# Kernel tuning notes

Hardware: AMD Instinct MI355X
Metric: run time of the kernel (lower is better)

## Reference

```python
import jax, jax.numpy as jnp
import numpy as np

EPS = 1e-10
COMMITMENT_COST = 0.25


def setup_inputs() -> dict:
    key = jax.random.key(0)
    k1, k2 = jax.random.split(key)
    inputs = jax.random.normal(k1, (64, 64, 32, 32), dtype=jnp.float32)
    # nn.init.uniform_(weight, -1.0, 1.0)
    embeddings = jax.random.uniform(k2, (1024, 64), dtype=jnp.float32, minval=-1.0, maxval=1.0)
    return {"inputs": inputs, "embeddings": embeddings}


def reference(inputs, embeddings):
    B, C, H, W = inputs.shape  # C == embedding_dim
    K = embeddings.shape[0]
    x = jnp.transpose(inputs, (0, 2, 3, 1)).reshape(-1, C)  # [N, D]
    d = (jnp.sum(x * x, axis=1, keepdims=True)
         - 2.0 * (x @ embeddings.T)
         + jnp.sum(embeddings * embeddings, axis=1))  # [N, K]
    idx = jnp.argmin(d, axis=1)  # [N]
    # one-hot @ embeddings == gather
    q = jnp.take(embeddings, idx, axis=0)  # [N, D]
    x4 = x.reshape(B, H, W, C)
    q4 = q.reshape(B, H, W, C)
    e_latent = jnp.mean((jax.lax.stop_gradient(q4) - x4) ** 2)
    q_latent = jnp.mean((q4 - jax.lax.stop_gradient(x4)) ** 2)
    loss = q_latent + COMMITMENT_COST * e_latent
    # straight-through estimator
    st = x4 + jax.lax.stop_gradient(q4 - x4)
    # avg_probs = mean of one-hot encodings == normalized histogram
    n = idx.shape[0]
    avg_probs = jnp.zeros((K,), dtype=jnp.float32).at[idx].add(1.0) / n
    perplexity = jnp.exp(-jnp.sum(avg_probs * jnp.log(avg_probs + EPS)))
    quantized = jnp.transpose(st, (0, 3, 1, 2))
    return quantized, loss, perplexity
```

## Files before the change

### kernel.cpp

```cpp
#include <hip/hip_runtime.h>

#define N_TOTAL   65536
#define HW_SZ     1024
#define CDIM      64
#define K_CODES   1024
#define OUT_ELEMS 4194304
#define QT        128
#define NCT       (K_CODES / 16)
#define TAU       0.004f


typedef __attribute__((ext_vector_type(8))) short short8;
typedef __attribute__((ext_vector_type(4))) float f32x4;

__device__ __forceinline__ unsigned short f2bf(float x) {
    unsigned u = __float_as_uint(x);
    return (unsigned short)((u + 0x7FFFu + ((u >> 16) & 1u)) >> 16);
}
__device__ __forceinline__ float bf2f(unsigned short h) {
    return __uint_as_float(((unsigned)h) << 16);
}
__device__ __forceinline__ void gload_lds16(const void* g, void* l) {
    __builtin_amdgcn_global_load_lds(
        (const __attribute__((address_space(1))) void*)g,
        (__attribute__((address_space(3))) void*)l, 16, 0, 0);
}

__global__ void k_prep(const float* __restrict__ emb, float* __restrict__ enorm,
                       short* __restrict__ btab, unsigned int* __restrict__ hist) {
    int gid = blockIdx.x * 256 + threadIdx.x;
    int r  = gid >> 4;
    int d0 = (gid & 15) * 4;
    float4 v = *(const float4*)(emb + gid * 4);
    float s = v.x * v.x + v.y * v.y + v.z * v.z + v.w * v.w;
#pragma unroll
    for (int off = 1; off < 16; off <<= 1) s += __shfl_xor(s, off, 64);
    if ((gid & 15) == 0) enorm[r] = s;

    float vv[4] = {v.x, v.y, v.z, v.w};
    short h[4], l[4];
#pragma unroll
    for (int j = 0; j < 4; ++j) {
        unsigned short hh = f2bf(vv[j]);
        h[j] = (short)hh;
        l[j] = (short)f2bf(vv[j] - bf2f(hh));
    }
    int base = (r >> 4) * 2048 + (d0 >> 5) * 1024
             + ((((d0 >> 3) & 3) * 16 + (r & 15)) * 8) + (d0 & 7);
    *(short4*)&btab[base]       = make_short4(h[0], h[1], h[2], h[3]);
    *(short4*)&btab[base + 512] = make_short4(l[0], l[1], l[2], l[3]);

    if (gid < K_CODES) hist[gid] = 0u;
}

__global__ __launch_bounds__(256, 2)
void k_argmin(const float* __restrict__ x, const float* __restrict__ emb,
              const short* __restrict__ btab, const float* __restrict__ enorm,
              unsigned int* __restrict__ hist, float* __restrict__ partials,
              float* __restrict__ out) {
    __shared__ __align__(16) float ens[K_CODES];
    __shared__ float xnorm[QT];
    __shared__ float rd1[QT];
    __shared__ float rd2[QT];
    __shared__ int   ri[QT];
    __shared__ int   flist[QT];
    __shared__ __align__(16) float xqf[CDIM];
    __shared__ __align__(16) float tile[64 * 72];
    __shared__ float wdd[4];
    __shared__ int   wii[4];
    __shared__ float spw[2];
    __shared__ int   nflag;

    const int tid  = threadIdx.x;
    const int lane = tid & 63;
    const int w    = tid >> 6;
    const int quad = lane >> 4;
    const int col  = lane & 15;

    const int n0  = blockIdx.x * QT;
    const int b   = n0 >> 10;
    const int hw0 = n0 & 1023;

    gload_lds16(&enorm[tid * 4], (void*)&ens[tid * 4]);

    const float* xb = x + b * (CDIM * HW_SZ) + hw0 + col;
    short8 afr[2][2][2];
#pragma unroll
    for (int rt = 0; rt < 2; ++rt) {
        float nloc = 0.f;
#pragma unroll
        for (int kc = 0; kc < 2; ++kc) {
#pragma unroll
            for (int j = 0; j < 8; ++j) {
                int c = (kc * 4 + quad) * 8 + j;
                float v = xb[c * HW_SZ + w * 32 + rt * 16];
                unsigned short hh = f2bf(v);
                afr[rt][kc][0][j] = (short)hh;
                afr[rt][kc][1][j] = (short)f2bf(v - bf2f(hh));
                nloc = __builtin_fmaf(v, v, nloc);
            }
        }
        nloc += __shfl_xor(nloc, 16, 64);
        nloc += __shfl_xor(nloc, 32, 64);
        if (quad == 0) xnorm[w * 32 + rt * 16 + col] = nloc;
    }
    __syncthreads();

    float d1[8], d2[8];
    int   i1[8];
#pragma unroll
    for (int t = 0; t < 8; ++t) { d1[t] = 3.4e38f; d2[t] = 3.4e38f; i1[t] = 0; }

    const short* bl = btab + lane * 8;

    short8 B0[2][2], B1[2][2], B2[2][2], B3[2][2];
    auto LDB = [&](short8 (&B)[2][2], int ct) {
        const short8* p = (const short8*)(bl + ct * 2048);
        B[0][0] = p[0];
        B[0][1] = p[64];
        B[1][0] = p[128];
        B[1][1] = p[192];
    };
    auto COMP = [&](short8 (&B)[2][2], int ct) {
        const int   mycode = ct * 16 + col;
        const float en     = ens[mycode];
#pragma unroll
        for (int rt = 0; rt < 2; ++rt) {
            f32x4 acc = {0.f, 0.f, 0.f, 0.f};
            acc = __builtin_amdgcn_mfma_f32_16x16x32_bf16(afr[rt][0][1], B[0][0], acc, 0, 0, 0);
            acc = __builtin_amdgcn_mfma_f32_16x16x32_bf16(afr[rt][0][0], B[0][1], acc, 0, 0, 0);
            acc = __builtin_amdgcn_mfma_f32_16x16x32_bf16(afr[rt][0][0], B[0][0], acc, 0, 0, 0);
            acc = __builtin_amdgcn_mfma_f32_16x16x32_bf16(afr[rt][1][1], B[1][0], acc, 0, 0, 0);
            acc = __builtin_amdgcn_mfma_f32_16x16x32_bf16(afr[rt][1][0], B[1][1], acc, 0, 0, 0);
            acc = __builtin_amdgcn_mfma_f32_16x16x32_bf16(afr[rt][1][0], B[1][0], acc, 0, 0, 0);
#pragma unroll
            for (int reg = 0; reg < 4; ++reg) {
                int t = rt * 4 + reg;
                float d   = __builtin_fmaf(acc[reg], -2.f, en);
                float d1o = d1[t];
                d2[t] = __builtin_amdgcn_fmed3f(d, d1o, d2[t]);
                d1[t] = fminf(d, d1o);
                i1[t] = (d < d1o) ? mycode : i1[t];
            }
        }
    };

    LDB(B0, 0); LDB(B1, 1); LDB(B2, 2); LDB(B3, 3);
    for (int ct = 0; ct < 60; ct += 4) {
        COMP(B0, ct    ); LDB(B0, ct + 4);
        COMP(B1, ct + 1); LDB(B1, ct + 5);
        COMP(B2, ct + 2); LDB(B2, ct + 6);
        COMP(B3, ct + 3); LDB(B3, ct + 7);
    }
    COMP(B0, 60); COMP(B1, 61); COMP(B2, 62); COMP(B3, 63);

#pragma unroll
    for (int t = 0; t < 8; ++t) {
        float a1 = d1[t], a2 = d2[t];
        int ai = i1[t];
#pragma unroll
        for (int off = 1; off < 16; off <<= 1) {
            float o1 = __shfl_xor(a1, off, 64);
            float o2 = __shfl_xor(a2, off, 64);
            int   oi = __shfl_xor(ai, off, 64);
            if (o1 < a1 || (o1 == a1 && oi < ai)) {
                float loser = a1; a2 = fminf(fminf(a2, o2), loser); a1 = o1; ai = oi;
            } else {
                a2 = fminf(fminf(a2, o2), o1);
            }
        }
        d1[t] = a1; d2[t] = a2; i1[t] = ai;
    }

    if (tid == 0) nflag = 0;
    if (col == 0) {
#pragma unroll
        for (int rt = 0; rt < 2; ++rt)
#pragma unroll
            for (int reg = 0; reg < 4; ++reg) {
                int t = rt * 4 + reg;
                int m = w * 32 + rt * 16 + quad * 4 + reg;
                rd1[m] = d1[t];
                rd2[m] = d2[t];
                ri [m] = i1[t];
            }
    }
    __syncthreads();

    if (tid < QT) {
        if (rd2[tid] - rd1[tid] < TAU) {
            int slot = atomicAdd(&nflag, 1);
            flist[slot] = tid;
        }
    }
    __syncthreads();

    for (int f = 0; f < nflag; ++f) {
        const int q = flist[f];
        if (tid < CDIM) xqf[tid] = x[b * (CDIM * HW_SZ) + tid * HW_SZ + hw0 + q];
        __syncthreads();
        float dm = 3.4e38f; int im = 0;
#pragma unroll
        for (int cd = 0; cd < 4; ++cd) {
            const int k = tid + cd * 256;
            const float4* er = (const float4*)(emb + k * CDIM);
            const float4* xr = (const float4*)xqf;
            float dot = 0.f;
#pragma unroll
            for (int c4 = 0; c4 < 16; ++c4) {
                float4 e = er[c4], xv = xr[c4];
                dot += e.x * xv.x + e.y * xv.y + e.z * xv.z + e.w * xv.w;
            }
            float d = ens[k] - 2.f * dot;
            if (d < dm) { dm = d; im = k; }
        }
#pragma unroll
        for (int off = 1; off < 64; off <<= 1) {
            float od = __shfl_xor(dm, off, 64);
            int   oi = __shfl_xor(im, off, 64);
            if (od < dm || (od == dm && oi < im)) { dm = od; im = oi; }
        }
        if (lane == 0) { wdd[w] = dm; wii[w] = im; }
        __syncthreads();
        if (tid == 0) {
            float bd = wdd[0]; int bi = wii[0];
#pragma unroll
            for (int ww = 1; ww < 4; ++ww)
                if (wdd[ww] < bd || (wdd[ww] == bd && wii[ww] < bi)) { bd = wdd[ww]; bi = wii[ww]; }
            rd1[q] = bd; ri[q] = bi;
        }
        __syncthreads();
    }

    if (tid < QT) {
        int ai = ri[tid];
        atomicAdd(&hist[ai], 1u);
        float sp = rd1[tid] + xnorm[tid];
#pragma unroll
        for (int off = 32; off; off >>= 1) sp += __shfl_down(sp, off, 64);
        if (lane == 0) spw[tid >> 6] = sp;
    }
    __syncthreads();
    if (tid == 0) partials[blockIdx.x] = spw[0] + spw[1];

#pragma unroll
    for (int h = 0; h < 2; ++h) {
        {
            int q = tid >> 2, j = tid & 3;
            int code = ri[h * 64 + q];
            int ct = code >> 4, cl = code & 15;
            int kc = j >> 1;
            int qa = (2 * j) & 3, qb = (2 * j + 1) & 3;
            const short* tb = btab + ct * 2048 + kc * 1024;
            short8 hi0 = *(const short8*)&tb[(qa * 16 + cl) * 8];
            short8 hi1 = *(const short8*)&tb[(qb * 16 + cl) * 8];
            short8 lo0 = *(const short8*)&tb[512 + (qa * 16 + cl) * 8];
            short8 lo1 = *(const short8*)&tb[512 + (qb * 16 + cl) * 8];
            float* dst = &tile[q * 72 + j * 16];
#pragma unroll
            for (int k = 0; k < 8; ++k) {
                dst[k]     = bf2f((unsigned short)hi0[k]) + bf2f((unsigned short)lo0[k]);
                dst[8 + k] = bf2f((unsigned short)hi1[k]) + bf2f((unsigned short)lo1[k]);
            }
        }
        __syncthreads();
        {
            int c = tid >> 2;
            float* ob = out + b * (CDIM * HW_SZ) + c * HW_SZ + hw0 + h * 64;
#pragma unroll
            for (int p = 0; p < 4; ++p) {
                int q = ((tid & 3) + p * 4) * 4;
                float4 v;
                v.x = tile[(q + 0) * 72 + c];
                v.y = tile[(q + 1) * 72 + c];
                v.z = tile[(q + 2) * 72 + c];
                v.w = tile[(q + 3) * 72 + c];
                *(float4*)&ob[q] = v;
            }
        }
        if (h == 0) __syncthreads();
    }
}

__global__ void k_final(const float* __restrict__ partials,
                        const unsigned int* __restrict__ hist,
                        float* __restrict__ out) {
    int tid = threadIdx.x;
    float ss = 0.f;
#pragma unroll
    for (int i = 0; i < 2; ++i) ss += partials[i * 256 + tid];
    float s = 0.f;
#pragma unroll
    for (int i = 0; i < 4; ++i) {
        float p = (float)hist[i * 256 + tid] * (1.0f / 65536.0f);
        s += p * logf(p + 1e-10f);
    }
    __shared__ float fin[8];
#pragma unroll
    for (int off = 32; off; off >>= 1) {
        ss += __shfl_down(ss, off, 64);
        s  += __shfl_down(s, off, 64);
    }
    if ((tid & 63) == 0) { fin[tid >> 6] = ss; fin[4 + (tid >> 6)] = s; }
    __syncthreads();
    if (tid == 0) {
        float sse = fin[0] + fin[1] + fin[2] + fin[3];
        float ent = fin[4] + fin[5] + fin[6] + fin[7];
        out[OUT_ELEMS]     = 1.25f * sse * (1.0f / (float)OUT_ELEMS);
        out[OUT_ELEMS + 1] = expf(-ent);
    }
}

extern "C" void kernel_launch(void* const* d_in, const int* in_sizes, int n_in,
                              void* d_out, int out_size, void* d_ws, size_t ws_size,
                              hipStream_t stream) {
    const float* x   = (const float*)d_in[0];
    const float* emb = (const float*)d_in[1];
    float* out = (float*)d_out;
    char* ws = (char*)d_ws;
    float*        enorm    = (float*)(ws);
    unsigned int* hist     = (unsigned int*)(ws + 4096);
    float*        partials = (float*)(ws + 8192);
    short*        btab     = (short*)(ws + 12288);

    k_prep  <<<64, 256, 0, stream>>>(emb, enorm, btab, hist);
    k_argmin<<<N_TOTAL / QT, 256, 0, stream>>>(x, emb, btab, enorm, hist, partials, out);
    k_final <<<1, 256, 0, stream>>>(partials, hist, out);
}
```

Measured before the change: 143.9 us.

## Double the query tile and stage codebook chunks in LDS via async loads

Each block now handles 256 query vectors instead of 128, so the codebook is streamed half as many times overall. The bf16 hi/lo codebook is brought into LDS in four chunks with double-buffered global_load_lds, and B fragments are read from LDS rather than straight from global/L2. The epilogue tile reuses the staging buffer, and the final reduction is adjusted for 256 blocks. The costs are a 128KB LDS footprint, one block per CU, more accumulator registers per thread, and fewer blocks (256), which may leave some CUs underused.

```diff
diff --git a/kernel.cpp b/kernel.cpp
--- a/kernel.cpp
+++ b/kernel.cpp
@@ -5,8 +5,8 @@
 #define CDIM      64
 #define K_CODES   1024
 #define OUT_ELEMS 4194304
-#define QT        128
-#define NCT       (K_CODES / 16)
+#define QT        256
+#define NCHUNK    4
 #define TAU       0.004f
 
 
@@ -53,11 +53,12 @@
     if (gid < K_CODES) hist[gid] = 0u;
 }
 
-__global__ __launch_bounds__(256, 2)
+__global__ __launch_bounds__(256, 1)
 void k_argmin(const float* __restrict__ x, const float* __restrict__ emb,
               const short* __restrict__ btab, const float* __restrict__ enorm,
               unsigned int* __restrict__ hist, float* __restrict__ partials,
               float* __restrict__ out) {
+    __shared__ __align__(16) short bufs[2][16 * 2048];
     __shared__ __align__(16) float ens[K_CODES];
     __shared__ float xnorm[QT];
     __shared__ float rd1[QT];
@@ -65,11 +66,11 @@
     __shared__ int   ri[QT];
     __shared__ int   flist[QT];
     __shared__ __align__(16) float xqf[CDIM];
-    __shared__ __align__(16) float tile[64 * 72];
     __shared__ float wdd[4];
     __shared__ int   wii[4];
-    __shared__ float spw[2];
+    __shared__ float spw[4];
     __shared__ int   nflag;
+    float* tile = (float*)bufs;
 
     const int tid  = threadIdx.x;
     const int lane = tid & 63;
@@ -81,19 +82,29 @@
     const int b   = n0 >> 10;
     const int hw0 = n0 & 1023;
 
+    auto stage_async = [&](int c, int bsel) {
+        const short* src = btab + c * (16 * 2048);
+#pragma unroll
+        for (int i = 0; i < 16; ++i) {
+            int idx = i * 256 + tid;
+            gload_lds16(&src[idx * 8], (void*)&bufs[bsel][idx * 8]);
+        }
+    };
+
+    stage_async(0, 0);
     gload_lds16(&enorm[tid * 4], (void*)&ens[tid * 4]);
 
     const float* xb = x + b * (CDIM * HW_SZ) + hw0 + col;
-    short8 afr[2][2][2];
-#pragma unroll
-    for (int rt = 0; rt < 2; ++rt) {
+    short8 afr[4][2][2];
+#pragma unroll
+    for (int rt = 0; rt < 4; ++rt) {
         float nloc = 0.f;
 #pragma unroll
         for (int kc = 0; kc < 2; ++kc) {
 #pragma unroll
             for (int j = 0; j < 8; ++j) {
-                int c = (kc * 4 + quad) * 8 + j;
-                float v = xb[c * HW_SZ + w * 32 + rt * 16];
+                int c0 = (kc * 4 + quad) * 8 + j;
+                float v = xb[c0 * HW_SZ + w * 64 + rt * 16];
                 unsigned short hh = f2bf(v);
                 afr[rt][kc][0][j] = (short)hh;
                 afr[rt][kc][1][j] = (short)f2bf(v - bf2f(hh));
@@ -102,60 +113,54 @@
         }
         nloc += __shfl_xor(nloc, 16, 64);
         nloc += __shfl_xor(nloc, 32, 64);
-        if (quad == 0) xnorm[w * 32 + rt * 16 + col] = nloc;
-    }
-    __syncthreads();
-
-    float d1[8], d2[8];
-    int   i1[8];
-#pragma unroll
-    for (int t = 0; t < 8; ++t) { d1[t] = 3.4e38f; d2[t] = 3.4e38f; i1[t] = 0; }
-
-    const short* bl = btab + lane * 8;
-
-    short8 B0[2][2], B1[2][2], B2[2][2], B3[2][2];
-    auto LDB = [&](short8 (&B)[2][2], int ct) {
-        const short8* p = (const short8*)(bl + ct * 2048);
-        B[0][0] = p[0];
-        B[0][1] = p[64];
-        B[1][0] = p[128];
-        B[1][1] = p[192];
-    };
-    auto COMP = [&](short8 (&B)[2][2], int ct) {
-        const int   mycode = ct * 16 + col;
-        const float en     = ens[mycode];
-#pragma unroll
-        for (int rt = 0; rt < 2; ++rt) {
-            f32x4 acc = {0.f, 0.f, 0.f, 0.f};
-            acc = __builtin_amdgcn_mfma_f32_16x16x32_bf16(afr[rt][0][1], B[0][0], acc, 0, 0, 0);
-            acc = __builtin_amdgcn_mfma_f32_16x16x32_bf16(afr[rt][0][0], B[0][1], acc, 0, 0, 0);
-            acc = __builtin_amdgcn_mfma_f32_16x16x32_bf16(afr[rt][0][0], B[0][0], acc, 0, 0, 0);
-            acc = __builtin_amdgcn_mfma_f32_16x16x32_bf16(afr[rt][1][1], B[1][0], acc, 0, 0, 0);
-            acc = __builtin_amdgcn_mfma_f32_16x16x32_bf16(afr[rt][1][0], B[1][1], acc, 0, 0, 0);
-            acc = __builtin_amdgcn_mfma_f32_16x16x32_bf16(afr[rt][1][0], B[1][0], acc, 0, 0, 0);
-#pragma unroll
-            for (int reg = 0; reg < 4; ++reg) {
-                int t = rt * 4 + reg;
-                float d   = __builtin_fmaf(acc[reg], -2.f, en);
-                float d1o = d1[t];
-                d2[t] = __builtin_amdgcn_fmed3f(d, d1o, d2[t]);
-                d1[t] = fminf(d, d1o);
-                i1[t] = (d < d1o) ? mycode : i1[t];
-            }
-        }
-    };
-
-    LDB(B0, 0); LDB(B1, 1); LDB(B2, 2); LDB(B3, 3);
-    for (int ct = 0; ct < 60; ct += 4) {
-        COMP(B0, ct    ); LDB(B0, ct + 4);
-        COMP(B1, ct + 1); LDB(B1, ct + 5);
-        COMP(B2, ct + 2); LDB(B2, ct + 6);
-        COMP(B3, ct + 3); LDB(B3, ct + 7);
-    }
-    COMP(B0, 60); COMP(B1, 61); COMP(B2, 62); COMP(B3, 63);
-
-#pragma unroll
-    for (int t = 0; t < 8; ++t) {
+        if (quad == 0) xnorm[w * 64 + rt * 16 + col] = nloc;
+    }
+
+    float d1[16], d2[16];
+    int   i1[16];
+#pragma unroll
+    for (int t = 0; t < 16; ++t) { d1[t] = 3.4e38f; d2[t] = 3.4e38f; i1[t] = 0; }
+
+    __syncthreads();
+
+    for (int c = 0; c < NCHUNK; ++c) {
+        if (c + 1 < NCHUNK) stage_async(c + 1, (c + 1) & 1);
+        const short* bs = &bufs[c & 1][0];
+        const int cbase = c * 256;
+#pragma unroll 4
+        for (int ctl = 0; ctl < 16; ++ctl) {
+            const short* fp = bs + ctl * 2048 + lane * 8;
+            short8 B00 = *(const short8*)(fp);
+            short8 B01 = *(const short8*)(fp + 512);
+            short8 B10 = *(const short8*)(fp + 1024);
+            short8 B11 = *(const short8*)(fp + 1536);
+            const int   mycode = cbase + ctl * 16 + col;
+            const float en     = ens[mycode];
+#pragma unroll
+            for (int rt = 0; rt < 4; ++rt) {
+                f32x4 acc = {0.f, 0.f, 0.f, 0.f};
+                acc = __builtin_amdgcn_mfma_f32_16x16x32_bf16(afr[rt][0][1], B00, acc, 0, 0, 0);
+                acc = __builtin_amdgcn_mfma_f32_16x16x32_bf16(afr[rt][0][0], B01, acc, 0, 0, 0);
+                acc = __builtin_amdgcn_mfma_f32_16x16x32_bf16(afr[rt][0][0], B00, acc, 0, 0, 0);
+                acc = __builtin_amdgcn_mfma_f32_16x16x32_bf16(afr[rt][1][1], B10, acc, 0, 0, 0);
+                acc = __builtin_amdgcn_mfma_f32_16x16x32_bf16(afr[rt][1][0], B11, acc, 0, 0, 0);
+                acc = __builtin_amdgcn_mfma_f32_16x16x32_bf16(afr[rt][1][0], B10, acc, 0, 0, 0);
+#pragma unroll
+                for (int reg = 0; reg < 4; ++reg) {
+                    int t = rt * 4 + reg;
+                    float d   = __builtin_fmaf(acc[reg], -2.f, en);
+                    float d1o = d1[t];
+                    d2[t] = __builtin_amdgcn_fmed3f(d, d1o, d2[t]);
+                    d1[t] = fminf(d, d1o);
+                    i1[t] = (d < d1o) ? mycode : i1[t];
+                }
+            }
+        }
+        __syncthreads();
+    }
+
+#pragma unroll
+    for (int t = 0; t < 16; ++t) {
         float a1 = d1[t], a2 = d2[t];
         int ai = i1[t];
 #pragma unroll
@@ -175,11 +180,11 @@
     if (tid == 0) nflag = 0;
     if (col == 0) {
 #pragma unroll
-        for (int rt = 0; rt < 2; ++rt)
+        for (int rt = 0; rt < 4; ++rt)
 #pragma unroll
             for (int reg = 0; reg < 4; ++reg) {
                 int t = rt * 4 + reg;
-                int m = w * 32 + rt * 16 + quad * 4 + reg;
+                int m = w * 64 + rt * 16 + quad * 4 + reg;
                 rd1[m] = d1[t];
                 rd2[m] = d2[t];
                 ri [m] = i1[t];
@@ -232,19 +237,19 @@
         __syncthreads();
     }
 
-    if (tid < QT) {
+    {
         int ai = ri[tid];
         atomicAdd(&hist[ai], 1u);
         float sp = rd1[tid] + xnorm[tid];
 #pragma unroll
         for (int off = 32; off; off >>= 1) sp += __shfl_down(sp, off, 64);
-        if (lane == 0) spw[tid >> 6] = sp;
-    }
-    __syncthreads();
-    if (tid == 0) partials[blockIdx.x] = spw[0] + spw[1];
-
-#pragma unroll
-    for (int h = 0; h < 2; ++h) {
+        if (lane == 0) spw[w] = sp;
+    }
+    __syncthreads();
+    if (tid == 0) partials[blockIdx.x] = spw[0] + spw[1] + spw[2] + spw[3];
+
+#pragma unroll
+    for (int h = 0; h < 4; ++h) {
         {
             int q = tid >> 2, j = tid & 3;
             int code = ri[h * 64 + q];
@@ -278,7 +283,7 @@
                 *(float4*)&ob[q] = v;
             }
         }
-        if (h == 0) __syncthreads();
+        if (h < 3) __syncthreads();
     }
 }
 
@@ -286,9 +291,7 @@
                         const unsigned int* __restrict__ hist,
                         float* __restrict__ out) {
     int tid = threadIdx.x;
-    float ss = 0.f;
-#pragma unroll
-    for (int i = 0; i < 2; ++i) ss += partials[i * 256 + tid];
+    float ss = partials[tid];
     float s = 0.f;
 #pragma unroll
     for (int i = 0; i < 4; ++i) {
```

New measurement: 132.3 us. -8.0%, faster.
